# Kernel optimization log

Hardware: AMD Instinct MI355X
Metric: run time of the kernel (lower is better)

## Reference

```python
import jax, jax.numpy as jnp
import numpy as np

N_EMBD = 1024
N_HEAD = 16
B, T = 8, 1024

def setup_inputs() -> dict:
    key = jax.random.key(0)
    ks = jax.random.split(key, 5)
    s = 0.02
    return {
        'x': jax.random.normal(ks[0], (B, T, N_EMBD), dtype=jnp.float32),
        'w_attn': jax.random.normal(ks[1], (N_EMBD, 3 * N_EMBD), dtype=jnp.float32) * s,
        'b_attn': jax.random.normal(ks[2], (3 * N_EMBD,), dtype=jnp.float32) * s,
        'w_proj': jax.random.normal(ks[3], (N_EMBD, N_EMBD), dtype=jnp.float32) * s,
        'b_proj': jax.random.normal(ks[4], (N_EMBD,), dtype=jnp.float32) * s,
    }

def reference(x, w_attn, b_attn, w_proj, b_proj):
    Bb, Tt, C = x.shape
    hd = C // N_HEAD  # head dim
    qkv = x @ w_attn + b_attn                      # [B,T,3C]
    q, k, v = jnp.split(qkv, 3, axis=2)
    # [B,T,C] -> [B,H,T,hd]
    def to_heads(t):
        return t.reshape(Bb, Tt, N_HEAD, hd).transpose(0, 2, 1, 3)
    q, k, v = to_heads(q), to_heads(k), to_heads(v)
    scale = 1.0 / jnp.sqrt(jnp.asarray(hd, dtype=x.dtype))
    att = jnp.einsum('bhqd,bhkd->bhqk', q, k) * scale  # [B,H,T,T]
    causal = jnp.tril(jnp.ones((Tt, Tt), dtype=bool))  # [T,T]
    att = jnp.where(causal[None, None, :, :], att, -jnp.inf)
    att = jax.nn.softmax(att, axis=-1)
    y = jnp.einsum('bhqk,bhkd->bhqd', att, v)          # [B,H,T,hd]
    y = y.transpose(0, 2, 1, 3).reshape(Bb, Tt, C)
    y = y @ w_proj + b_proj
    return y
```

## Files before the change

### kernel.cpp

```cpp
#include <hip/hip_runtime.h>
#include <stdint.h>

#define N_EMBD 1024
#define NHEAD  16
#define HDIM   64
#define BATCH  8
#define SEQ    1024
#define MROWS  (BATCH*SEQ)

typedef __bf16 bf16x8 __attribute__((ext_vector_type(8)));
typedef float  f32x4  __attribute__((ext_vector_type(4)));

__device__ inline unsigned short f2bf(float f) {
  uint32_t u = __float_as_uint(f);
  u += 0x7FFFu + ((u >> 16) & 1u);
  return (unsigned short)(u >> 16);
}

__device__ inline f32x4 mfma_bf16(bf16x8 a, bf16x8 b, f32x4 c) {
  return __builtin_amdgcn_mfma_f32_16x16x32_bf16(a, b, c, 0, 0, 0);
}

__device__ inline void gload_lds16(const unsigned short* g, unsigned short* l) {
  __builtin_amdgcn_global_load_lds(
      (const __attribute__((address_space(1))) void*)g,
      (__attribute__((address_space(3))) void*)l,
      16, 0, 0);
}

#define DSB __builtin_amdgcn_sched_barrier(0)
#define BARRIER __builtin_amdgcn_s_barrier()
#define VMC(n) asm volatile("s_waitcnt vmcnt(" #n ")" ::: "memory")
#define LGKM0 asm volatile("s_waitcnt lgkmcnt(0)" ::: "memory"); DSB

__global__ __launch_bounds__(256) void cast_f32_bf16(
    const float* __restrict__ in, unsigned short* __restrict__ out, int n) {
  int i = (blockIdx.x * 256 + threadIdx.x) * 4;
  if (i >= n) return;
  float4 v = *(const float4*)(in + i);
  ushort4 o;
  o.x = f2bf(v.x); o.y = f2bf(v.y); o.z = f2bf(v.z); o.w = f2bf(v.w);
  *(ushort4*)(out + i) = o;
}

__global__ __launch_bounds__(256) void transpose_cast2(
    const float* __restrict__ wa, unsigned short* __restrict__ oa,
    const float* __restrict__ wp, unsigned short* __restrict__ op) {
  __shared__ unsigned short tile[64 * 72];
  const int K = 1024;
  int bx = blockIdx.x;
  const float* in; unsigned short* out; int N;
  if (bx < 48) { in = wa; out = oa; N = 3072; }
  else         { in = wp; out = op; N = 1024; bx -= 48; }
  int k0 = blockIdx.y * 64, n0 = bx * 64;
  int t = threadIdx.x;
  {
    int col = (t & 15) * 4;
#pragma unroll
    for (int it = 0; it < 4; ++it) {
      int row = (t >> 4) + it * 16;
      float4 v = *(const float4*)(in + (size_t)(k0 + row) * N + n0 + col);
      ushort4 o;
      o.x = f2bf(v.x); o.y = f2bf(v.y); o.z = f2bf(v.z); o.w = f2bf(v.w);
      *(ushort4*)&tile[row * 72 + col] = o;
    }
  }
  __syncthreads();
  {
    int kcol = (t & 7) * 8;
#pragma unroll
    for (int it = 0; it < 2; ++it) {
      int nrow = (t >> 3) + it * 32;
      alignas(16) unsigned short tmp[8];
#pragma unroll
      for (int j = 0; j < 8; ++j) tmp[j] = tile[(kcol + j) * 72 + nrow];
      *(uint4*)(out + (size_t)(n0 + nrow) * K + k0 + kcol) = *(const uint4*)tmp;
    }
  }
}

#define GEMM98_CORE(A_, Bt_, NBN_)                                              \
  __shared__ unsigned short Asl[2][8192];                                       \
  __shared__ unsigned short Bsl[2][8192];                                       \
  const int tid = threadIdx.x;                                                  \
  const int l = tid & 63, w = tid >> 6;                                         \
  const int wr = w >> 1, wc = w & 1;                                            \
  const int g = l >> 4, fr = l & 15;                                            \
  const int nwg = 64 * (NBN_);                                                  \
  int bid = blockIdx.x;                                                         \
  int swzb = (bid & 7) * (nwg >> 3) + (bid >> 3);      \
  const int n0 = (swzb % (NBN_)) * 128;                                         \
  const int m0 = (swzb / (NBN_)) * 128;                                         \
  f32x4 acc[4][4];                                                              \
  _Pragma("unroll") for (int i = 0; i < 4; ++i)                                 \
    _Pragma("unroll") for (int j = 0; j < 4; ++j)                               \
      _Pragma("unroll") for (int r = 0; r < 4; ++r) acc[i][j][r] = 0.0f;        \
  const int rr = tid >> 3;                                                      \
  const int cs = ((tid & 7) * 16) ^ ((rr & 7) << 4);                            \
  const char* srcA[4]; const char* srcB[4];                                     \
  _Pragma("unroll") for (int c = 0; c < 4; ++c) {                               \
    srcA[c] = (const char*)(A_) + (size_t)(m0 + c * 32 + rr) * 2048 + cs;       \
    srcB[c] = (const char*)(Bt_) + (size_t)(n0 + c * 32 + rr) * 2048 + cs;      \
  }                                                                             \
  const int ldso = tid * 8;                                         \
  const int arow = (wr * 64 + fr) * 128;                                        \
  const int brow = (wc * 64 + fr) * 128;                                        \
  int colk[2];                                                                  \
  colk[0] = (g * 16) ^ ((fr & 7) << 4);                                         \
  colk[1] = (64 + g * 16) ^ ((fr & 7) << 4);                                    \
  _Pragma("unroll") for (int c = 0; c < 4; ++c)                                 \
    gload_lds16((const unsigned short*)(srcA[c]), &Asl[0][ldso + c * 2048]);    \
  _Pragma("unroll") for (int c = 0; c < 4; ++c)                                 \
    gload_lds16((const unsigned short*)(srcB[c]), &Bsl[0][ldso + c * 2048]);    \
  _Pragma("unroll") for (int c = 0; c < 4; ++c)                                 \
    gload_lds16((const unsigned short*)(srcA[c] + 128), &Asl[1][ldso + c * 2048]);\
  _Pragma("unroll") for (int c = 0; c < 4; ++c)                                 \
    gload_lds16((const unsigned short*)(srcB[c] + 128), &Bsl[1][ldso + c * 2048]);\
  for (int kt = 0; kt < 16; ++kt) {                                             \
    const int cur = kt & 1;                                                     \
    if (kt < 15) { VMC(8); } else { VMC(0); }                                   \
    DSB; BARRIER; DSB;                                                          \
    _Pragma("unroll") for (int ks = 0; ks < 2; ++ks) {                          \
      bf16x8 av[4], bv[4];                                                      \
      _Pragma("unroll") for (int m = 0; m < 4; ++m)                             \
        av[m] = *(const bf16x8*)((const char*)&Asl[cur][0] + arow +             \
                                 m * 16 * 128 + colk[ks]);                      \
      _Pragma("unroll") for (int n = 0; n < 4; ++n)                             \
        bv[n] = *(const bf16x8*)((const char*)&Bsl[cur][0] + brow +             \
                                 n * 16 * 128 + colk[ks]);                      \
      _Pragma("unroll") for (int n = 0; n < 4; ++n)                             \
        _Pragma("unroll") for (int m = 0; m < 4; ++m)                           \
          acc[m][n] = mfma_bf16(av[m], bv[n], acc[m][n]);                       \
    }                                                                           \
    LGKM0; BARRIER; DSB;                                                        \
    if (kt < 14) {                                                              \
      const int ko = (kt + 2) * 128;                                            \
      _Pragma("unroll") for (int c = 0; c < 4; ++c)                             \
        gload_lds16((const unsigned short*)(srcA[c] + ko),                      \
                    &Asl[cur][ldso + c * 2048]);                                \
      _Pragma("unroll") for (int c = 0; c < 4; ++c)                             \
        gload_lds16((const unsigned short*)(srcB[c] + ko),                      \
                    &Bsl[cur][ldso + c * 2048]);                                \
    }                                                                           \
  }

__global__ __launch_bounds__(256) void gemm_qkv(
    const unsigned short* __restrict__ A, const unsigned short* __restrict__ Bt,
    const float* __restrict__ bias,
    unsigned short* __restrict__ Qo, unsigned short* __restrict__ Ko,
    unsigned short* __restrict__ VTo) {
  GEMM98_CORE(A, Bt, 24)
#pragma unroll
  for (int i = 0; i < 4; ++i) {
    int mb = m0 + wr * 64 + i * 16 + 4 * g;
    int bidx = mb >> 10;
    int t = mb & 1023;
#pragma unroll
    for (int j = 0; j < 4; ++j) {
      int n = n0 + wc * 64 + j * 16 + fr;
      float bv2 = bias[n];
      int part = n >> 10;
      int nn2 = n & 1023;
      int h = nn2 >> 6, d = nn2 & 63;
      if (part == 2) {
        alignas(8) unsigned short pk[4];
#pragma unroll
        for (int r = 0; r < 4; ++r) pk[r] = f2bf(acc[i][j][r] + bv2);
        *(ushort4*)&VTo[((size_t)(bidx * NHEAD + h) * HDIM + d) * SEQ + t] =
            *(const ushort4*)pk;
      } else {
        unsigned short* dst = (part == 0) ? Qo : Ko;
        float scl = (part == 0) ? 0.125f : 1.0f;
        size_t base = ((size_t)(bidx * NHEAD + h) * SEQ + t) * HDIM + d;
#pragma unroll
        for (int r = 0; r < 4; ++r)
          dst[base + (size_t)r * HDIM] = f2bf((acc[i][j][r] + bv2) * scl);
      }
    }
  }
}

__global__ __launch_bounds__(256) void gemm_proj(
    const unsigned short* __restrict__ A, const unsigned short* __restrict__ Bt,
    const float* __restrict__ bias, float* __restrict__ Out) {
  GEMM98_CORE(A, Bt, 8)
#pragma unroll
  for (int i = 0; i < 4; ++i) {
    int mb = m0 + wr * 64 + i * 16 + 4 * g;
#pragma unroll
    for (int j = 0; j < 4; ++j) {
      int n = n0 + wc * 64 + j * 16 + fr;
      float bv2 = bias[n];
#pragma unroll
      for (int r = 0; r < 4; ++r)
        Out[(size_t)(mb + r) * N_EMBD + n] = acc[i][j][r] + bv2;
    }
  }
}

__global__ __launch_bounds__(256) void attn_kernel(
    const unsigned short* __restrict__ Q, const unsigned short* __restrict__ Kv,
    const unsigned short* __restrict__ VT, unsigned short* __restrict__ Y) {
  __shared__ unsigned short Kt[2][4096];
  __shared__ unsigned short Vt[2][4096];
  __shared__ unsigned short p_lds[4 * 32 * 72];
  __shared__ float smx[4][32];
  int tid = threadIdx.x, l = tid & 63, w = tid >> 6;
  int bid = blockIdx.x;
  int swz = (bid & 7) * 64 + (bid >> 3);
  int bh = swz >> 2;
  int pairIdx = swz & 3;
  int b = bh >> 4, h = bh & 15;
  const unsigned short* Qb = Q + (size_t)bh * SEQ * HDIM;
  const char* Kc = (const char*)(Kv + (size_t)bh * SEQ * HDIM);
  const char* Vc = (const char*)(VT + (size_t)bh * HDIM * SEQ);
  unsigned short* pw = &p_lds[w * 32 * 72];
  const int g = l >> 4;
  const int fr = l & 15;

  const int P0 = tid * 16, P1 = tid * 16 + 4096;
  const int r0 = P0 >> 7, r1 = P1 >> 7;
  const int s0 = (P0 & 127) ^ ((r0 & 7) << 4);
  const int s1 = (P1 & 127) ^ ((r1 & 7) << 4);
  const char* Kg0 = Kc + r0 * 128 + s0;
  const char* Kg1 = Kc + r1 * 128 + s1;
  const char* Vg0 = Vc + (size_t)r0 * 2048 + s0;
  const char* Vg1 = Vc + (size_t)r1 * 2048 + s1;

  const int bc = (16 * g) ^ ((l & 7) << 4);

  for (int part = 0; part < 2; ++part) {
    const int qt = (part == 0) ? pairIdx : 7 - pairIdx;
    const int q0 = qt * 128;
    const int wq = q0 + w * 32;

    bf16x8 aq[2][2];
#pragma unroll
    for (int i = 0; i < 2; ++i)
#pragma unroll
      for (int ik = 0; ik < 2; ++ik)
        aq[i][ik] = *(const bf16x8*)&Qb[(size_t)(wq + i * 16 + fr) * HDIM + ik * 32 + 8 * g];

    float mrun[2], lpart[2];
    mrun[0] = mrun[1] = 0.0f;
    lpart[0] = lpart[1] = 0.0f;
    f32x4 acc_o[2][4];
#pragma unroll
    for (int i = 0; i < 2; ++i)
#pragma unroll
      for (int jd = 0; jd < 4; ++jd)
#pragma unroll
        for (int r = 0; r < 4; ++r) acc_o[i][jd][r] = 0.0f;

    const int n_it = (q0 + 128) >> 6;

    gload_lds16((const unsigned short*)(Kg0), &Kt[0][P0 >> 1]);
    gload_lds16((const unsigned short*)(Kg1), &Kt[0][P1 >> 1]);
    gload_lds16((const unsigned short*)(Vg0), &Vt[0][P0 >> 1]);
    gload_lds16((const unsigned short*)(Vg1), &Vt[0][P1 >> 1]);

    for (int it = 0; it < n_it; ++it) {
      const int kv0 = it << 6;
      const int cur = it & 1;
      if (it + 1 < n_it) {
        const int nx = kv0 + 64;
        gload_lds16((const unsigned short*)(Kg0 + nx * 128), &Kt[cur ^ 1][P0 >> 1]);
        gload_lds16((const unsigned short*)(Kg1 + nx * 128), &Kt[cur ^ 1][P1 >> 1]);
        gload_lds16((const unsigned short*)(Vg0 + nx * 2),   &Vt[cur ^ 1][P0 >> 1]);
        gload_lds16((const unsigned short*)(Vg1 + nx * 2),   &Vt[cur ^ 1][P1 >> 1]);
        VMC(4);
      } else {
        VMC(0);
      }
      DSB; BARRIER; DSB;

      const char* Kbuf = (const char*)Kt[cur];
      const char* Vbuf = (const char*)Vt[cur];

      f32x4 s2[2][4];
#pragma unroll
      for (int i = 0; i < 2; ++i)
#pragma unroll
        for (int j = 0; j < 4; ++j)
#pragma unroll
          for (int r = 0; r < 4; ++r) s2[i][j][r] = 0.0f;

      __builtin_amdgcn_s_setprio(1);
#pragma unroll
      for (int ik = 0; ik < 2; ++ik) {
#pragma unroll
        for (int j = 0; j < 4; ++j) {
          bf16x8 bk = *(const bf16x8*)(Kbuf + (j * 16 + fr) * 128 + (bc ^ (ik << 6)));
#pragma unroll
          for (int i = 0; i < 2; ++i) s2[i][j] = mfma_bf16(bk, aq[i][ik], s2[i][j]);
        }
      }
      __builtin_amdgcn_s_setprio(0);

      bool need_mask = (kv0 + 63) > wq;
      if (need_mask) {
#pragma unroll
        for (int i = 0; i < 2; ++i) {
          int q = wq + i * 16 + fr;
#pragma unroll
          for (int j = 0; j < 4; ++j)
#pragma unroll
            for (int r = 0; r < 4; ++r) {
              int kv = kv0 + j * 16 + 4 * g + r;
              if (kv > q) s2[i][j][r] = -3.0e38f;
            }
        }
      }

      float pmloc[2];
#pragma unroll
      for (int i = 0; i < 2; ++i) {
        float m01 = fmaxf(fmaxf(s2[i][0][0], s2[i][0][1]), fmaxf(s2[i][0][2], s2[i][0][3]));
        float m11 = fmaxf(fmaxf(s2[i][1][0], s2[i][1][1]), fmaxf(s2[i][1][2], s2[i][1][3]));
        float m21 = fmaxf(fmaxf(s2[i][2][0], s2[i][2][1]), fmaxf(s2[i][2][2], s2[i][2][3]));
        float m31 = fmaxf(fmaxf(s2[i][3][0], s2[i][3][1]), fmaxf(s2[i][3][2], s2[i][3][3]));
        pmloc[i] = fmaxf(fmaxf(m01, m11), fmaxf(m21, m31));
      }
      bool ok = (pmloc[0] <= mrun[0] + 8.0f) && (pmloc[1] <= mrun[1] + 8.0f);
      if (!__all(ok)) {
#pragma unroll
        for (int i = 0; i < 2; ++i) {
          float mm = pmloc[i];
          mm = fmaxf(mm, __shfl_xor(mm, 16, 64));
          mm = fmaxf(mm, __shfl_xor(mm, 32, 64));
          float mn = fmaxf(mrun[i], mm);
          float sc = __expf(mrun[i] - mn);
          mrun[i] = mn;
          lpart[i] *= sc;
          if (g == 0) smx[w][i * 16 + fr] = sc;
        }
        asm volatile("s_waitcnt lgkmcnt(0)" ::: "memory");
#pragma unroll
        for (int i = 0; i < 2; ++i)
#pragma unroll
          for (int r = 0; r < 4; ++r) {
            float sc = smx[w][i * 16 + 4 * g + r];
#pragma unroll
            for (int jd = 0; jd < 4; ++jd) acc_o[i][jd][r] *= sc;
          }
      }

#pragma unroll
      for (int i = 0; i < 2; ++i) {
#pragma unroll
        for (int j = 0; j < 4; ++j) {
          float p0 = __expf(s2[i][j][0] - mrun[i]);
          float p1 = __expf(s2[i][j][1] - mrun[i]);
          float p2 = __expf(s2[i][j][2] - mrun[i]);
          float p3 = __expf(s2[i][j][3] - mrun[i]);
          lpart[i] += (p0 + p1) + (p2 + p3);
          uint2 pk2;
          asm("v_cvt_pk_bf16_f32 %0, %1, %2" : "=v"(pk2.x) : "v"(p0), "v"(p1));
          asm("v_cvt_pk_bf16_f32 %0, %1, %2" : "=v"(pk2.y) : "v"(p2), "v"(p3));
          *(uint2*)&pw[(i * 16 + fr) * 72 + j * 16 + 4 * g] = pk2;
        }
      }

      __builtin_amdgcn_s_setprio(1);
#pragma unroll
      for (int ik2 = 0; ik2 < 2; ++ik2) {
        bf16x8 ap[2];
#pragma unroll
        for (int i = 0; i < 2; ++i)
          ap[i] = *(const bf16x8*)&pw[(i * 16 + fr) * 72 + ik2 * 32 + 8 * g];
#pragma unroll
        for (int jd = 0; jd < 4; ++jd) {
          bf16x8 bv = *(const bf16x8*)(Vbuf + (jd * 16 + fr) * 128 + (bc ^ (ik2 << 6)));
#pragma unroll
          for (int i = 0; i < 2; ++i) acc_o[i][jd] = mfma_bf16(ap[i], bv, acc_o[i][jd]);
        }
      }
      __builtin_amdgcn_s_setprio(0);

      asm volatile("s_waitcnt lgkmcnt(0)" ::: "memory");
      DSB; BARRIER; DSB;
    }

#pragma unroll
    for (int i = 0; i < 2; ++i) {
      float t = lpart[i];
      t += __shfl_xor(t, 16, 64);
      t += __shfl_xor(t, 32, 64);
      if (g == 0) smx[w][i * 16 + fr] = t;
    }
    asm volatile("s_waitcnt lgkmcnt(0)" ::: "memory");
#pragma unroll
    for (int i = 0; i < 2; ++i)
#pragma unroll
      for (int r = 0; r < 4; ++r) {
        float inv = 1.0f / smx[w][i * 16 + 4 * g + r];
        int q = wq + i * 16 + 4 * g + r;
#pragma unroll
        for (int jd = 0; jd < 4; ++jd)
          Y[((size_t)b * SEQ + q) * N_EMBD + h * HDIM + jd * 16 + fr] =
              f2bf(acc_o[i][jd][r] * inv);
      }
  }
}

extern "C" void kernel_launch(void* const* d_in, const int* in_sizes, int n_in,
                              void* d_out, int out_size, void* d_ws, size_t ws_size,
                              hipStream_t stream) {
  (void)in_sizes; (void)n_in; (void)out_size; (void)ws_size;
  const float* x      = (const float*)d_in[0];
  const float* w_attn = (const float*)d_in[1];
  const float* b_attn = (const float*)d_in[2];
  const float* w_proj = (const float*)d_in[3];
  const float* b_proj = (const float*)d_in[4];
  float* out = (float*)d_out;

  char* ws = (char*)d_ws;
  size_t off = 0;
  auto carve = [&](size_t bytes) -> char* {
    char* p = ws + off;
    off += (bytes + 255) & ~(size_t)255;
    return p;
  };
  unsigned short* xb     = (unsigned short*)carve((size_t)MROWS * N_EMBD * 2);
  unsigned short* wTattn = (unsigned short*)carve((size_t)3 * N_EMBD * N_EMBD * 2);
  unsigned short* wTproj = (unsigned short*)carve((size_t)N_EMBD * N_EMBD * 2);
  unsigned short* Qb     = (unsigned short*)carve((size_t)MROWS * N_EMBD * 2);
  unsigned short* Kb     = (unsigned short*)carve((size_t)MROWS * N_EMBD * 2);
  unsigned short* VTb    = (unsigned short*)carve((size_t)MROWS * N_EMBD * 2);
  unsigned short* Yb     = (unsigned short*)carve((size_t)MROWS * N_EMBD * 2);
  carve(4096);

  cast_f32_bf16<<<dim3(MROWS * N_EMBD / 1024), 256, 0, stream>>>(x, xb, MROWS * N_EMBD);
  transpose_cast2<<<dim3(64, 16), 256, 0, stream>>>(w_attn, wTattn, w_proj, wTproj);
  gemm_qkv<<<dim3(64 * 24), 256, 0, stream>>>(xb, wTattn, b_attn, Qb, Kb, VTb);
  attn_kernel<<<dim3(512), 256, 0, stream>>>(Qb, Kb, VTb, Yb);
  gemm_proj<<<dim3(64 * 8), 256, 0, stream>>>(Yb, wTproj, b_proj, out);
}
```

Measured before the change: 144.5 us.

## Replace double-buffered GEMM core with 4-slot K=32 ring and XCD-aware tiling

The GEMM mainloop moves from a 2-stage buffer with K=64 tiles to a 4-slot ring of K=32 tiles prefetched three stages ahead, so more global loads stay in flight while MFMAs run. Block-to-tile mapping is rewritten so each XCD gets a contiguous 8x8 patch of output tiles for better L2 reuse. Epilogue stores become nontemporal. The new LDS layout drops the XOR swizzle, which may cause bank conflicts on fragment reads, and a barrier now sits between the LDS reads and the MFMAs.

```diff
diff --git a/kernel.cpp b/kernel.cpp
--- a/kernel.cpp
+++ b/kernel.cpp
@@ -10,6 +10,7 @@
 
 typedef __bf16 bf16x8 __attribute__((ext_vector_type(8)));
 typedef float  f32x4  __attribute__((ext_vector_type(4)));
+typedef unsigned short u16x4 __attribute__((ext_vector_type(4)));
 
 __device__ inline unsigned short f2bf(float f) {
   uint32_t u = __float_as_uint(f);
@@ -79,69 +80,53 @@
   }
 }
 
-#define GEMM98_CORE(A_, Bt_, NBN_)                                              \
-  __shared__ unsigned short Asl[2][8192];                                       \
-  __shared__ unsigned short Bsl[2][8192];                                       \
+
+#define RING32_DECL(A_, Bt_)                                                    \
+  const char* srcA[2]; const char* srcB[2];                                     \
+  _Pragma("unroll") for (int c = 0; c < 2; ++c) {                               \
+    const int row_ = c * 64 + (tid >> 2);                                       \
+    const int col_ = (tid & 3) * 16;                                            \
+    srcA[c] = (const char*)(A_) + (size_t)(m0 + row_) * 2048 + col_;            \
+    srcB[c] = (const char*)(Bt_) + (size_t)(n0 + row_) * 2048 + col_;           \
+  }
+
+#define RING32_STAGE(slot, ktile)                                               \
+  _Pragma("unroll") for (int c = 0; c < 2; ++c) {                               \
+    gload_lds16((const unsigned short*)(srcA[c] + (ktile) * 64),                \
+                &Asl[slot][c * 2048 + tid * 8]);                                \
+    gload_lds16((const unsigned short*)(srcB[c] + (ktile) * 64),                \
+                &Bsl[slot][c * 2048 + tid * 8]);                                \
+  }
+
+#define RING32_CORE(A_, Bt_)                                                    \
+  __shared__ unsigned short Asl[4][4096];                                       \
+  __shared__ unsigned short Bsl[4][4096];                                       \
   const int tid = threadIdx.x;                                                  \
   const int l = tid & 63, w = tid >> 6;                                         \
   const int wr = w >> 1, wc = w & 1;                                            \
   const int g = l >> 4, fr = l & 15;                                            \
-  const int nwg = 64 * (NBN_);                                                  \
-  int bid = blockIdx.x;                                                         \
-  int swzb = (bid & 7) * (nwg >> 3) + (bid >> 3);      \
-  const int n0 = (swzb % (NBN_)) * 128;                                         \
-  const int m0 = (swzb / (NBN_)) * 128;                                         \
   f32x4 acc[4][4];                                                              \
   _Pragma("unroll") for (int i = 0; i < 4; ++i)                                 \
     _Pragma("unroll") for (int j = 0; j < 4; ++j)                               \
       _Pragma("unroll") for (int r = 0; r < 4; ++r) acc[i][j][r] = 0.0f;        \
-  const int rr = tid >> 3;                                                      \
-  const int cs = ((tid & 7) * 16) ^ ((rr & 7) << 4);                            \
-  const char* srcA[4]; const char* srcB[4];                                     \
-  _Pragma("unroll") for (int c = 0; c < 4; ++c) {                               \
-    srcA[c] = (const char*)(A_) + (size_t)(m0 + c * 32 + rr) * 2048 + cs;       \
-    srcB[c] = (const char*)(Bt_) + (size_t)(n0 + c * 32 + rr) * 2048 + cs;      \
-  }                                                                             \
-  const int ldso = tid * 8;                                         \
-  const int arow = (wr * 64 + fr) * 128;                                        \
-  const int brow = (wc * 64 + fr) * 128;                                        \
-  int colk[2];                                                                  \
-  colk[0] = (g * 16) ^ ((fr & 7) << 4);                                         \
-  colk[1] = (64 + g * 16) ^ ((fr & 7) << 4);                                    \
-  _Pragma("unroll") for (int c = 0; c < 4; ++c)                                 \
-    gload_lds16((const unsigned short*)(srcA[c]), &Asl[0][ldso + c * 2048]);    \
-  _Pragma("unroll") for (int c = 0; c < 4; ++c)                                 \
-    gload_lds16((const unsigned short*)(srcB[c]), &Bsl[0][ldso + c * 2048]);    \
-  _Pragma("unroll") for (int c = 0; c < 4; ++c)                                 \
-    gload_lds16((const unsigned short*)(srcA[c] + 128), &Asl[1][ldso + c * 2048]);\
-  _Pragma("unroll") for (int c = 0; c < 4; ++c)                                 \
-    gload_lds16((const unsigned short*)(srcB[c] + 128), &Bsl[1][ldso + c * 2048]);\
-  for (int kt = 0; kt < 16; ++kt) {                                             \
-    const int cur = kt & 1;                                                     \
-    if (kt < 15) { VMC(8); } else { VMC(0); }                                   \
-    DSB; BARRIER; DSB;                                                          \
-    _Pragma("unroll") for (int ks = 0; ks < 2; ++ks) {                          \
-      bf16x8 av[4], bv[4];                                                      \
+  RING32_DECL(A_, Bt_)                                                          \
+  const int abase = wr * 4096 + fr * 64 + g * 16;                               \
+  const int bbase = wc * 4096 + fr * 64 + g * 16;                               \
+  RING32_STAGE(0, 0) RING32_STAGE(1, 1) RING32_STAGE(2, 2)                      \
+  for (int kt = 0; kt < 32; ++kt) {                                             \
+    const int s = kt & 3;                                                       \
+    const int stg = (kt + 3 > 31) ? 31 : (kt + 3);                              \
+    RING32_STAGE((kt + 3) & 3, stg)                                             \
+    VMC(12); DSB; BARRIER; DSB;                                                 \
+    bf16x8 av[4], bv[4];                                                        \
+    _Pragma("unroll") for (int m = 0; m < 4; ++m)                               \
+      av[m] = *(const bf16x8*)((const char*)&Asl[s][0] + abase + m * 1024);     \
+    _Pragma("unroll") for (int n = 0; n < 4; ++n)                               \
+      bv[n] = *(const bf16x8*)((const char*)&Bsl[s][0] + bbase + n * 1024);     \
+    LGKM0; BARRIER; DSB;                                                        \
+    _Pragma("unroll") for (int n = 0; n < 4; ++n)                               \
       _Pragma("unroll") for (int m = 0; m < 4; ++m)                             \
-        av[m] = *(const bf16x8*)((const char*)&Asl[cur][0] + arow +             \
-                                 m * 16 * 128 + colk[ks]);                      \
-      _Pragma("unroll") for (int n = 0; n < 4; ++n)                             \
-        bv[n] = *(const bf16x8*)((const char*)&Bsl[cur][0] + brow +             \
-                                 n * 16 * 128 + colk[ks]);                      \
-      _Pragma("unroll") for (int n = 0; n < 4; ++n)                             \
-        _Pragma("unroll") for (int m = 0; m < 4; ++m)                           \
-          acc[m][n] = mfma_bf16(av[m], bv[n], acc[m][n]);                       \
-    }                                                                           \
-    LGKM0; BARRIER; DSB;                                                        \
-    if (kt < 14) {                                                              \
-      const int ko = (kt + 2) * 128;                                            \
-      _Pragma("unroll") for (int c = 0; c < 4; ++c)                             \
-        gload_lds16((const unsigned short*)(srcA[c] + ko),                      \
-                    &Asl[cur][ldso + c * 2048]);                                \
-      _Pragma("unroll") for (int c = 0; c < 4; ++c)                             \
-        gload_lds16((const unsigned short*)(srcB[c] + ko),                      \
-                    &Bsl[cur][ldso + c * 2048]);                                \
-    }                                                                           \
+        acc[m][n] = mfma_bf16(av[m], bv[n], acc[m][n]);                         \
   }
 
 __global__ __launch_bounds__(256) void gemm_qkv(
@@ -149,7 +134,14 @@
     const float* __restrict__ bias,
     unsigned short* __restrict__ Qo, unsigned short* __restrict__ Ko,
     unsigned short* __restrict__ VTo) {
-  GEMM98_CORE(A, Bt, 24)
+  const int bid = blockIdx.x;
+  const int xcd = bid & 7;
+  const int local = bid >> 3;
+  const int nchunk = local >> 6;
+  const int rem = local & 63;
+  const int m0 = (xcd * 8 + (rem >> 3)) * 128;
+  const int n0 = (nchunk * 8 + (rem & 7)) * 128;
+  RING32_CORE(A, Bt)
 #pragma unroll
   for (int i = 0; i < 4; ++i) {
     int mb = m0 + wr * 64 + i * 16 + 4 * g;
@@ -163,18 +155,21 @@
       int nn2 = n & 1023;
       int h = nn2 >> 6, d = nn2 & 63;
       if (part == 2) {
-        alignas(8) unsigned short pk[4];
-#pragma unroll
-        for (int r = 0; r < 4; ++r) pk[r] = f2bf(acc[i][j][r] + bv2);
-        *(ushort4*)&VTo[((size_t)(bidx * NHEAD + h) * HDIM + d) * SEQ + t] =
-            *(const ushort4*)pk;
+        u16x4 pk;
+        pk[0] = f2bf(acc[i][j][0] + bv2);
+        pk[1] = f2bf(acc[i][j][1] + bv2);
+        pk[2] = f2bf(acc[i][j][2] + bv2);
+        pk[3] = f2bf(acc[i][j][3] + bv2);
+        __builtin_nontemporal_store(
+            pk, (u16x4*)&VTo[((size_t)(bidx * NHEAD + h) * HDIM + d) * SEQ + t]);
       } else {
         unsigned short* dst = (part == 0) ? Qo : Ko;
         float scl = (part == 0) ? 0.125f : 1.0f;
         size_t base = ((size_t)(bidx * NHEAD + h) * SEQ + t) * HDIM + d;
 #pragma unroll
         for (int r = 0; r < 4; ++r)
-          dst[base + (size_t)r * HDIM] = f2bf((acc[i][j][r] + bv2) * scl);
+          __builtin_nontemporal_store(f2bf((acc[i][j][r] + bv2) * scl),
+                                      &dst[base + (size_t)r * HDIM]);
       }
     }
   }
@@ -183,7 +178,12 @@
 __global__ __launch_bounds__(256) void gemm_proj(
     const unsigned short* __restrict__ A, const unsigned short* __restrict__ Bt,
     const float* __restrict__ bias, float* __restrict__ Out) {
-  GEMM98_CORE(A, Bt, 8)
+  const int bid = blockIdx.x;
+  const int xcd = bid & 7;
+  const int local = bid >> 3;
+  const int m0 = (xcd * 8 + (local >> 3)) * 128;
+  const int n0 = (local & 7) * 128;
+  RING32_CORE(A, Bt)
 #pragma unroll
   for (int i = 0; i < 4; ++i) {
     int mb = m0 + wr * 64 + i * 16 + 4 * g;
@@ -193,7 +193,8 @@
       float bv2 = bias[n];
 #pragma unroll
       for (int r = 0; r < 4; ++r)
-        Out[(size_t)(mb + r) * N_EMBD + n] = acc[i][j][r] + bv2;
+        __builtin_nontemporal_store(acc[i][j][r] + bv2,
+                                    &Out[(size_t)(mb + r) * N_EMBD + n]);
     }
   }
 }
@@ -432,7 +433,7 @@
 
   cast_f32_bf16<<<dim3(MROWS * N_EMBD / 1024), 256, 0, stream>>>(x, xb, MROWS * N_EMBD);
   transpose_cast2<<<dim3(64, 16), 256, 0, stream>>>(w_attn, wTattn, w_proj, wTproj);
-  gemm_qkv<<<dim3(64 * 24), 256, 0, stream>>>(xb, wTattn, b_attn, Qb, Kb, VTb);
+  gemm_qkv<<<dim3(1536), 256, 0, stream>>>(xb, wTattn, b_attn, Qb, Kb, VTb);
   attn_kernel<<<dim3(512), 256, 0, stream>>>(Qb, Kb, VTb, Yb);
-  gemm_proj<<<dim3(64 * 8), 256, 0, stream>>>(Yb, wTproj, b_proj, out);
-}
+  gemm_proj<<<dim3(512), 256, 0, stream>>>(Yb, wTproj, b_proj, out);
+}
```

Result: slower. 178.2 us (+23.3%).
